# Kernel tuning notes

Measured on AMD Instinct MI355X. Metric: run time of the kernel, lower is better.

The kernel has to match this reference:

```python
import jax, jax.numpy as jnp
import numpy as np

B, NIMG, H, W, C = 4, 4, 80, 80, 256
NH = 8
C1 = C // 8          # 32
CPH = C1 // NH       # 4 per-head conv channels
K2D = 4              # deformable attention sampling points
HD2 = C1 // NH       # 4 head dim for 2D deformable attention
INNER = 32           # 3D deformable attention inner dim
DSF = (2, 8, 8)
OSC = jnp.array([2.0, 8.0, 8.0], jnp.float32)


def _bilin2d(img, px, py):
    # img [B,C,H,W]; px,py [B,K] pixel coords -> [B,K,C], zero-padded outside
    Bb, Cc, Hh, Ww = img.shape
    x0 = jnp.floor(px); y0 = jnp.floor(py)
    wx = px - x0; wy = py - y0
    bidx = jnp.arange(Bb)[:, None]
    def g(yy, xx):
        valid = (xx >= 0) & (xx <= Ww - 1) & (yy >= 0) & (yy <= Hh - 1)
        xi = jnp.clip(xx, 0, Ww - 1).astype(jnp.int32)
        yi = jnp.clip(yy, 0, Hh - 1).astype(jnp.int32)
        return img[bidx, :, yi, xi] * valid[..., None]
    return (g(y0, x0) * ((1 - wy) * (1 - wx))[..., None]
          + g(y0, x0 + 1) * ((1 - wy) * wx)[..., None]
          + g(y0 + 1, x0) * (wy * (1 - wx))[..., None]
          + g(y0 + 1, x0 + 1) * (wy * wx)[..., None])


def _trilin(img, z, y, x):
    # img [B,C,D,H,W]; z,y,x [B,K] -> [B,K,C]
    Bb, Cc, Dd, Hh, Ww = img.shape
    z0 = jnp.floor(z); y0 = jnp.floor(y); x0 = jnp.floor(x)
    wz = z - z0; wy = y - y0; wx = x - x0
    bidx = jnp.arange(Bb)[:, None]
    def g(zz, yy, xx):
        valid = (zz >= 0) & (zz <= Dd - 1) & (yy >= 0) & (yy <= Hh - 1) & (xx >= 0) & (xx <= Ww - 1)
        zi = jnp.clip(zz, 0, Dd - 1).astype(jnp.int32)
        yi = jnp.clip(yy, 0, Hh - 1).astype(jnp.int32)
        xi = jnp.clip(xx, 0, Ww - 1).astype(jnp.int32)
        return img[bidx, :, zi, yi, xi] * valid[..., None]
    out = 0.
    for dz in (0., 1.):
        for dy in (0., 1.):
            for dx in (0., 1.):
                w = ((1 - wz) if dz == 0. else wz) * ((1 - wy) if dy == 0. else wy) * ((1 - wx) if dx == 0. else wx)
                out = out + g(z0 + dz, y0 + dy, x0 + dx) * w[..., None]
    return out


def _fwd(x, W_qkv, b_qkv, W_fc, b_fc, W_doff, b_doff, W_dep, b_dep, W_st, b_st,
         W_off2d, b_off2d, W_attw, b_attw, W_val, b_val, W_out2d, b_out2d,
         W_q3, b_q3, W_k3, b_k3, W_v3, b_v3, W_offA, b_offA, W_offB, b_offB,
         W_out3, b_out3, rate1, rate2, nimg):
    xb = jnp.transpose(x, (1, 0, 2))                       # [B, nHW, C]
    Bb = xb.shape[0]
    qkv = xb @ W_qkv + b_qkv                               # [B, nHW, 2*C1]
    # ---------- deformable-conv (ACMix) branch ----------
    f_all = qkv.reshape(Bb, nimg * H * W, 2 * NH, CPH).transpose(0, 2, 1, 3)
    f9 = jnp.einsum('oc,bcnk->bonk', W_fc, f_all) + b_fc[None, :, None, None]
    f_conv = f9.transpose(0, 3, 1, 2).reshape(Bb, 9 * CPH, nimg, H, W)
    fin = f_conv.transpose(0, 2, 1, 3, 4).reshape(Bb * nimg, 9 * CPH, H, W)
    off = jax.lax.conv_general_dilated(fin, W_doff, (1, 1), ((1, 1), (1, 1)),
          dimension_numbers=('NCHW', 'OIHW', 'NCHW')) + b_doff[None, :, None, None]
    off = off.reshape(Bb * nimg, 9, 2, H, W)               # (dy,dx) per 3x3 tap
    hh, ww = jnp.meshgrid(jnp.arange(H, dtype=jnp.float32), jnp.arange(W, dtype=jnp.float32), indexing='ij')
    tap = jnp.arange(9)
    ky = (tap // 3 - 1).astype(jnp.float32); kx = (tap % 3 - 1).astype(jnp.float32)
    py = hh[None, None] + ky[None, :, None, None] + off[:, :, 0]
    px = ww[None, None] + kx[None, :, None, None] + off[:, :, 1]
    samp = _bilin2d(fin, px.reshape(Bb * nimg, -1), py.reshape(Bb * nimg, -1))
    samp = samp.reshape(Bb * nimg, 9, H, W, 9 * CPH).transpose(0, 4, 1, 2, 3)
    sg = samp.reshape(Bb * nimg, CPH, 9, 9, H, W)          # [Bn, g, cin_pg, taps, H, W]
    wg = W_dep.reshape(CPH, 27, 9, 9)                      # [g, out_pg, cin_pg, taps]
    dep = jnp.einsum('bgikhw,goik->bgohw', sg, wg).reshape(Bb * nimg, 27 * CPH, H, W) + b_dep[None, :, None, None]
    oc = dep.reshape(Bb, nimg, 27 * CPH, H, W).transpose(0, 2, 1, 3, 4)
    st_in = oc.reshape(Bb, CPH, 27, nimg, H, W)
    st = jnp.einsum('bginhw,goi->bgonhw', st_in, W_st).reshape(Bb, C, nimg, H, W) + b_st[None, :, None, None, None]
    out_conv = st.transpose(2, 3, 4, 0, 1).reshape(nimg * H * W, Bb, C)
    # ---------- per-frame 2D deformable attention ----------
    qk = qkv.reshape(Bb, nimg, H, W, 2, C1)
    q2 = qk[..., 0, :].reshape(Bb * nimg, H, W, C1)
    k2 = qk[..., 1, :].reshape(Bb * nimg, H, W, C1)
    gy, gx = jnp.meshgrid(jnp.arange(H, dtype=jnp.float32) / (H - 1),
                          jnp.arange(W, dtype=jnp.float32) / (W - 1), indexing='ij')
    ref = jnp.stack([gx, gy], -1)                          # [H,W,2] normalized (x,y)
    off2 = (q2 @ W_off2d + b_off2d).reshape(Bb * nimg, H, W, NH, K2D, 2)
    attw = jax.nn.softmax((q2 @ W_attw + b_attw).reshape(Bb * nimg, H, W, NH, K2D), axis=-1)
    v2 = (k2 @ W_val + b_val).reshape(Bb * nimg, H, W, NH, HD2)
    vimg = v2.transpose(0, 3, 4, 1, 2).reshape(Bb * nimg * NH, HD2, H, W)
    loc = ref[None, :, :, None, None, :] + off2 / jnp.array([W, H], jnp.float32)
    ppx = (loc[..., 0] * (W - 1)).transpose(0, 3, 1, 2, 4).reshape(Bb * nimg * NH, H * W * K2D)
    ppy = (loc[..., 1] * (H - 1)).transpose(0, 3, 1, 2, 4).reshape(Bb * nimg * NH, H * W * K2D)
    s2 = _bilin2d(vimg, ppx, ppy).reshape(Bb * nimg, NH, H, W, K2D, HD2)
    a2 = jnp.einsum('bhwnk,bnhwkd->bhwnd', attw, s2).reshape(Bb * nimg, H, W, C1)
    a2 = (a2 @ W_out2d + b_out2d).reshape(Bb, nimg, H, W, C1)
    # faithful reproduction of the source's frame-concat bug: frames [0,0,1,...,nimg-2]
    idx = jnp.array([0] + list(range(nimg - 1)))
    x3 = a2[:, idx].transpose(0, 4, 1, 2, 3)               # [B, C1, nimg, H, W]
    # ---------- 3D deformable attention ----------
    q3 = jnp.einsum('oc,bcnhw->bonhw', W_q3, x3) + b_q3[None, :, None, None, None]
    hid = jax.lax.conv_general_dilated(q3, W_offA, DSF, ((1, 1), (1, 1), (1, 1)),
          dimension_numbers=('NCDHW', 'OIDHW', 'NCDHW')) + b_offA[None, :, None, None, None]
    hid = jax.nn.gelu(hid)
    off3 = jnp.einsum('oc,bcnhw->bonhw', W_offB, hid) + b_offB[None, :, None, None, None]
    off3 = jnp.tanh(off3) * OSC[None, :, None, None, None]
    npr, hpr, wpr = off3.shape[2], off3.shape[3], off3.shape[4]
    gz, gy2, gx2 = jnp.meshgrid(jnp.arange(npr, dtype=jnp.float32) * 2 + 0.5,
                                jnp.arange(hpr, dtype=jnp.float32) * 8 + 3.5,
                                jnp.arange(wpr, dtype=jnp.float32) * 8 + 3.5, indexing='ij')
    cz = (gz[None] + off3[:, 0]).reshape(Bb, -1)
    cy = (gy2[None] + off3[:, 1]).reshape(Bb, -1)
    cx = (gx2[None] + off3[:, 2]).reshape(Bb, -1)
    kf = jnp.einsum('oc,bcnhw->bonhw', W_k3, x3) + b_k3[None, :, None, None, None]
    vf = jnp.einsum('oc,bcnhw->bonhw', W_v3, x3) + b_v3[None, :, None, None, None]
    ks_ = _trilin(kf, cz, cy, cx)                          # [B, L, INNER]
    vs_ = _trilin(vf, cz, cy, cx)
    qf = q3.reshape(Bb, INNER, -1).transpose(0, 2, 1)      # [B, N, INNER]
    at = jax.nn.softmax(jnp.einsum('bnd,bld->bnl', qf, ks_) * (INNER ** -0.5), axis=-1)
    o3 = jnp.einsum('bnl,bld->bnd', at, vs_).transpose(0, 2, 1).reshape(Bb, INNER, nimg, H, W)
    o3 = jnp.einsum('oc,bcnhw->bonhw', W_out3, o3) + b_out3[None, :, None, None, None]
    xattn = o3.transpose(2, 3, 4, 0, 1).reshape(nimg * H * W, Bb, C)
    return rate1 * xattn + rate2 * out_conv


def _p(key, shape, s=0.02):
    return jax.random.normal(key, shape, jnp.float32) * s


def setup_inputs() -> dict:
    key = jax.random.key(0)
    ks = jax.random.split(key, 20)
    z = lambda *s: jnp.zeros(s, jnp.float32)
    return {
        'x': jax.random.normal(ks[0], (NIMG * H * W, B, C), jnp.float32),
        'W_qkv': _p(ks[1], (C, C // 4)), 'b_qkv': z(C // 4),
        'W_fc': _p(ks[2], (9, 2 * NH)), 'b_fc': z(9),
        'W_doff': _p(ks[3], (18, 9 * CPH, 3, 3), 0.01), 'b_doff': z(18),
        'W_dep': _p(ks[4], (27 * CPH, 9, 3, 3)), 'b_dep': z(27 * CPH),
        'W_st': _p(ks[5], (CPH, C // CPH, 27)), 'b_st': z(C),
        'W_off2d': _p(ks[6], (C1, NH * K2D * 2), 0.01), 'b_off2d': z(NH * K2D * 2),
        'W_attw': _p(ks[7], (C1, NH * K2D)), 'b_attw': z(NH * K2D),
        'W_val': _p(ks[8], (C1, C1)), 'b_val': z(C1),
        'W_out2d': _p(ks[9], (C1, C1)), 'b_out2d': z(C1),
        'W_q3': _p(ks[10], (INNER, C1)), 'b_q3': z(INNER),
        'W_k3': _p(ks[11], (INNER, C1)), 'b_k3': z(INNER),
        'W_v3': _p(ks[12], (INNER, C1)), 'b_v3': z(INNER),
        'W_offA': _p(ks[13], (INNER, INNER, 4, 10, 10), 0.01), 'b_offA': z(INNER),
        'W_offB': _p(ks[14], (3, INNER), 0.01), 'b_offB': z(3),
        'W_out3': _p(ks[15], (C, INNER)), 'b_out3': z(C),
        'rate1': jnp.full((1,), 0.5, jnp.float32),
        'rate2': jnp.full((1,), 0.5, jnp.float32),
        'nimg': NIMG,
    }


def reference(x, W_qkv, b_qkv, W_fc, b_fc, W_doff, b_doff, W_dep, b_dep, W_st, b_st,
              W_off2d, b_off2d, W_attw, b_attw, W_val, b_val, W_out2d, b_out2d,
              W_q3, b_q3, W_k3, b_k3, W_v3, b_v3, W_offA, b_offA, W_offB, b_offB,
              W_out3, b_out3, rate1, rate2, nimg):
    return _fwd(x, W_qkv, b_qkv, W_fc, b_fc, W_doff, b_doff, W_dep, b_dep, W_st, b_st,
                W_off2d, b_off2d, W_attw, b_attw, W_val, b_val, W_out2d, b_out2d,
                W_q3, b_q3, W_k3, b_k3, W_v3, b_v3, W_offA, b_offA, W_offB, b_offB,
                W_out3, b_out3, rate1, rate2, nimg)
```

## Files before the change

kernel.cpp:

```cpp
#include <hip/hip_runtime.h>
#include <math.h>

#define B_     4
#define NIMG_  4
#define H_     80
#define W_     80
#define C_     256
#define NH_    8
#define HW_    6400
#define NQ_    25600
#define NPIX_  102400
#define L3_    200

#define WS_QH   0u
#define WS_KH   3276800u
#define WS_V2   6553600u
#define WS_FIN2 9830400u
#define WS_OFF  3276800u
#define WS_A2   9830400u
#define WS_Q3   0u
#define WS_KF   3276800u
#define WS_VF   6553600u
#define WS_CRD  9830400u
#define WS_KS   9832800u
#define WS_VS   9858400u
#define WS_O3   3276800u

__global__ __launch_bounds__(256) void k_qkv(const float* __restrict__ x,
        const float* __restrict__ Wq, const float* __restrict__ bq,
        float* __restrict__ qh, float* __restrict__ kh) {
    __shared__ __align__(16) float xs[32][256];
    int t = threadIdx.x;
    int row0 = blockIdx.x * 32;
    for (int it = 0; it < 8; ++it) {
        int idx = t + it * 256;
        int r = idx >> 6;
        int f4 = idx & 63;
        int row = row0 + r;
        int b = row / NQ_, n = row % NQ_;
        const float4* src = (const float4*)(x + ((size_t)n * B_ + b) * C_);
        ((float4*)&xs[r][0])[f4] = src[f4];
    }
    __syncthreads();
    int j = t & 63;
    int rbase = (t >> 6) * 8;
    float acc[8];
    #pragma unroll
    for (int r = 0; r < 8; ++r) acc[r] = 0.f;
    for (int c4 = 0; c4 < 64; ++c4) {
        float w0 = Wq[(c4 * 4 + 0) * 64 + j];
        float w1 = Wq[(c4 * 4 + 1) * 64 + j];
        float w2 = Wq[(c4 * 4 + 2) * 64 + j];
        float w3 = Wq[(c4 * 4 + 3) * 64 + j];
        #pragma unroll
        for (int r = 0; r < 8; ++r) {
            float4 xv = ((const float4*)&xs[rbase + r][0])[c4];
            acc[r] += xv.x * w0 + xv.y * w1 + xv.z * w2 + xv.w * w3;
        }
    }
    float bias = bq[j];
    #pragma unroll
    for (int r = 0; r < 8; ++r) {
        int row = row0 + rbase + r;
        float vres = acc[r] + bias;
        if (j < 32) qh[(size_t)row * 32 + j] = vres;
        else        kh[(size_t)row * 32 + (j - 32)] = vres;
    }
}

__global__ __launch_bounds__(256) void k_fin_v2(const float* __restrict__ qh,
        const float* __restrict__ kh,
        const float* __restrict__ Wfc, const float* __restrict__ bfc,
        const float* __restrict__ Wval, const float* __restrict__ bval,
        float* __restrict__ fin2, float* __restrict__ v2) {
    __shared__ float WvalL[1024], WfcL[144], bfcL[9], bvalL[32];
    int t = threadIdx.x;
    for (int d = t; d < 1024; d += 256) WvalL[d] = Wval[d];
    if (t < 144) WfcL[t] = Wfc[t];
    if (t >= 160 && t < 169) bfcL[t - 160] = bfc[t - 160];
    if (t >= 192 && t < 224) bvalL[t - 192] = bval[t - 192];
    __syncthreads();
    int P = blockIdx.x * 256 + t;
    int b = P / NQ_, nq = P % NQ_;
    int n = nq / HW_, hw = nq % HW_;
    int bn = b * NIMG_ + n;
    float q[64];
    const float4* qp = (const float4*)(qh + (size_t)P * 32);
    const float4* kp = (const float4*)(kh + (size_t)P * 32);
    #pragma unroll
    for (int i = 0; i < 8; ++i) ((float4*)q)[i] = qp[i];
    #pragma unroll
    for (int i = 0; i < 8; ++i) ((float4*)q)[8 + i] = kp[i];
    float fo[36];
    #pragma unroll
    for (int k = 0; k < 4; ++k)
        #pragma unroll
        for (int o = 0; o < 9; ++o) fo[k * 9 + o] = bfcL[o];
    for (int c = 0; c < 16; ++c) {
        #pragma unroll
        for (int o = 0; o < 9; ++o) {
            float wv = WfcL[o * 16 + c];
            #pragma unroll
            for (int k = 0; k < 4; ++k) fo[k * 9 + o] += wv * q[c * 4 + k];
        }
    }
    float* fp = fin2 + ((size_t)bn * HW_ + hw) * 48;
    #pragma unroll
    for (int g = 0; g < 4; ++g) {
        ((float4*)fp)[g * 3 + 0] = make_float4(fo[g * 9 + 0], fo[g * 9 + 1], fo[g * 9 + 2], fo[g * 9 + 3]);
        ((float4*)fp)[g * 3 + 1] = make_float4(fo[g * 9 + 4], fo[g * 9 + 5], fo[g * 9 + 6], fo[g * 9 + 7]);
        ((float4*)fp)[g * 3 + 2] = make_float4(fo[g * 9 + 8], 0.f, 0.f, 0.f);
    }
    float vo[32];
    #pragma unroll
    for (int j = 0; j < 32; ++j) vo[j] = bvalL[j];
    for (int c = 0; c < 32; ++c) {
        float qc = q[32 + c];
        #pragma unroll
        for (int j = 0; j < 32; ++j) vo[j] += qc * WvalL[c * 32 + j];
    }
    float* vp = v2 + ((size_t)bn * HW_ + hw) * 32;
    #pragma unroll
    for (int i = 0; i < 8; ++i) ((float4*)vp)[i] = ((float4*)vo)[i];
}

__global__ __launch_bounds__(256) void k_offconv(const float* __restrict__ fin2,
        const float* __restrict__ Wdoff, const float* __restrict__ bdoff,
        float* __restrict__ off) {
    __shared__ float Wl[5832];
    int t = threadIdx.x;
    for (int d = t; d < 5832; d += 256) {
        int tap = d / 648, r = d % 648, c = r / 18, o = r % 18;
        Wl[d] = Wdoff[(o * 36 + c) * 9 + tap];
    }
    __syncthreads();
    int P = blockIdx.x * 256 + t;
    int bn = P / HW_, hw = P % HW_;
    int h = hw / W_, w = hw % W_;
    float acc[18];
    #pragma unroll
    for (int o = 0; o < 18; ++o) acc[o] = bdoff[o];
    for (int ky = 0; ky < 3; ++ky) {
        int hh = h + ky - 1;
        if (hh < 0 || hh >= H_) continue;
        for (int kx = 0; kx < 3; ++kx) {
            int ww = w + kx - 1;
            if (ww < 0 || ww >= W_) continue;
            int sp = hh * W_ + ww;
            const float4* base = (const float4*)(fin2 + ((size_t)bn * HW_ + sp) * 48);
            const float* wl = Wl + (ky * 3 + kx) * 648;
            #pragma unroll
            for (int g = 0; g < 4; ++g) {
                float4 p0 = base[g * 3 + 0], p1 = base[g * 3 + 1], p2 = base[g * 3 + 2];
                float vals[9] = {p0.x, p0.y, p0.z, p0.w, p1.x, p1.y, p1.z, p1.w, p2.x};
                #pragma unroll
                for (int idx = 0; idx < 9; ++idx) {
                    const float* w0 = wl + (g * 9 + idx) * 18;
                    float vv = vals[idx];
                    #pragma unroll
                    for (int o = 0; o < 18; ++o) acc[o] += vv * w0[o];
                }
            }
        }
    }
    float* op = off + (size_t)P * 18;
    #pragma unroll
    for (int o = 0; o < 18; ++o) op[o] = acc[o];
}

__global__ __launch_bounds__(256, 4) void k_depst(const float* __restrict__ fin2,
        const float* __restrict__ off, const float* __restrict__ Wdep,
        const float* __restrict__ bdep, const float* __restrict__ Wst,
        const float* __restrict__ bst, const float* __restrict__ rate2p,
        float* __restrict__ out) {
    __shared__ __align__(16) float wdepL[2268];
    __shared__ __align__(16) float wstL[1728];
    __shared__ float bdepL[27];
    __shared__ float bstL[64];
    int t = threadIdx.x;
    int bx = blockIdx.x;
    int u = (bx & 7) * 200 + (bx >> 3);
    int chunk = u >> 2, g = u & 3;
    for (int d = t; d < 2268; d += 256) {
        int k = d / 252, r2 = d % 252;
        int i = r2 / 28, o = r2 % 28;
        wdepL[d] = (o < 27) ? Wdep[(size_t)(g * 27 + o) * 81 + i * 9 + k] : 0.f;
    }
    for (int d = t; d < 1728; d += 256) {
        int i = d >> 6, o = d & 63;
        wstL[d] = Wst[g * 1728 + o * 27 + i];
    }
    if (t < 27) bdepL[t] = bdep[g * 27 + t];
    if (t >= 32 && t < 96) bstL[t - 32] = bst[g * 64 + (t - 32)];
    __syncthreads();
    int P = chunk * 256 + t;
    int bn = P / HW_, hw = P % HW_;
    int h = hw / W_, w = hw % W_;
    int b = bn >> 2, n = bn & 3;
    const float* finb = fin2 + (size_t)bn * (HW_ * 48) + g * 12;
    float2 offs[9];
    {
        const float2* op2 = (const float2*)(off + (size_t)P * 18);
        #pragma unroll
        for (int k = 0; k < 9; ++k) offs[k] = op2[k];
    }
    float acc[27];
    #pragma unroll
    for (int o = 0; o < 27; ++o) acc[o] = 0.f;
    float hf = (float)h, wf = (float)w;
    #pragma unroll 1
    for (int k = 0; k < 9; ++k) {
        float py = hf + (float)(k / 3 - 1) + offs[k].x;
        float px = wf + (float)(k % 3 - 1) + offs[k].y;
        float y0f = floorf(py), x0f = floorf(px);
        float wy = py - y0f, wx = px - x0f;
        float wy0 = 1.f - wy, wx0 = 1.f - wx;
        float vy0 = (y0f >= 0.f && y0f <= 79.f) ? 1.f : 0.f;
        float vy1 = (y0f >= -1.f && y0f <= 78.f) ? 1.f : 0.f;
        float vx0 = (x0f >= 0.f && x0f <= 79.f) ? 1.f : 0.f;
        float vx1 = (x0f >= -1.f && x0f <= 78.f) ? 1.f : 0.f;
        int yi0 = (int)fminf(fmaxf(y0f, 0.f), 79.f);
        int yi1 = (int)fminf(fmaxf(y0f + 1.f, 0.f), 79.f);
        int xi0 = (int)fminf(fmaxf(x0f, 0.f), 79.f);
        int xi1 = (int)fminf(fmaxf(x0f + 1.f, 0.f), 79.f);
        float w00 = wy0 * wx0 * vy0 * vx0;
        float w01 = wy0 * wx  * vy0 * vx1;
        float w10 = wy  * wx0 * vy1 * vx0;
        float w11 = wy  * wx  * vy1 * vx1;
        const float4* c00 = (const float4*)(finb + (size_t)(yi0 * W_ + xi0) * 48);
        const float4* c01 = (const float4*)(finb + (size_t)(yi0 * W_ + xi1) * 48);
        const float4* c10 = (const float4*)(finb + (size_t)(yi1 * W_ + xi0) * 48);
        const float4* c11 = (const float4*)(finb + (size_t)(yi1 * W_ + xi1) * 48);
        float s[9];
        {
            float4 p0 = c00[0], p1 = c00[1], p2 = c00[2];
            s[0] = w00 * p0.x; s[1] = w00 * p0.y; s[2] = w00 * p0.z; s[3] = w00 * p0.w;
            s[4] = w00 * p1.x; s[5] = w00 * p1.y; s[6] = w00 * p1.z; s[7] = w00 * p1.w;
            s[8] = w00 * p2.x;
        }
        {
            float4 p0 = c01[0], p1 = c01[1], p2 = c01[2];
            s[0] += w01 * p0.x; s[1] += w01 * p0.y; s[2] += w01 * p0.z; s[3] += w01 * p0.w;
            s[4] += w01 * p1.x; s[5] += w01 * p1.y; s[6] += w01 * p1.z; s[7] += w01 * p1.w;
            s[8] += w01 * p2.x;
        }
        {
            float4 p0 = c10[0], p1 = c10[1], p2 = c10[2];
            s[0] += w10 * p0.x; s[1] += w10 * p0.y; s[2] += w10 * p0.z; s[3] += w10 * p0.w;
            s[4] += w10 * p1.x; s[5] += w10 * p1.y; s[6] += w10 * p1.z; s[7] += w10 * p1.w;
            s[8] += w10 * p2.x;
        }
        {
            float4 p0 = c11[0], p1 = c11[1], p2 = c11[2];
            s[0] += w11 * p0.x; s[1] += w11 * p0.y; s[2] += w11 * p0.z; s[3] += w11 * p0.w;
            s[4] += w11 * p1.x; s[5] += w11 * p1.y; s[6] += w11 * p1.z; s[7] += w11 * p1.w;
            s[8] += w11 * p2.x;
        }
        const float* wk = wdepL + k * 252;
        #pragma unroll
        for (int i = 0; i < 9; ++i) {
            float si = s[i];
            const float4* rw = (const float4*)(wk + i * 28);
            float4 q0 = rw[0], q1 = rw[1], q2 = rw[2], q3v = rw[3];
            float4 q4 = rw[4], q5 = rw[5], q6 = rw[6];
            acc[0]  += si * q0.x;  acc[1]  += si * q0.y;  acc[2]  += si * q0.z;  acc[3]  += si * q0.w;
            acc[4]  += si * q1.x;  acc[5]  += si * q1.y;  acc[6]  += si * q1.z;  acc[7]  += si * q1.w;
            acc[8]  += si * q2.x;  acc[9]  += si * q2.y;  acc[10] += si * q2.z;  acc[11] += si * q2.w;
            acc[12] += si * q3v.x; acc[13] += si * q3v.y; acc[14] += si * q3v.z; acc[15] += si * q3v.w;
            acc[16] += si * q4.x;  acc[17] += si * q4.y;  acc[18] += si * q4.z;  acc[19] += si * q4.w;
            acc[20] += si * q5.x;  acc[21] += si * q5.y;  acc[22] += si * q5.z;  acc[23] += si * q5.w;
            acc[24] += si * q6.x;  acc[25] += si * q6.y;  acc[26] += si * q6.z;
        }
    }
    #pragma unroll
    for (int i = 0; i < 27; ++i) acc[i] += bdepL[i];
    float r2v = rate2p[0];
    float* ob = out + ((size_t)(n * HW_ + hw) * B_ + b) * C_ + g * 64;
    #pragma unroll 1
    for (int half = 0; half < 2; ++half) {
        float ro[32];
        #pragma unroll
        for (int o = 0; o < 32; ++o) ro[o] = bstL[half * 32 + o];
        #pragma unroll
        for (int i = 0; i < 27; ++i) {
            float ai = acc[i];
            const float4* rw = (const float4*)(wstL + i * 64 + half * 32);
            #pragma unroll
            for (int j = 0; j < 8; ++j) {
                float4 wv = rw[j];
                ro[j * 4 + 0] += ai * wv.x;
                ro[j * 4 + 1] += ai * wv.y;
                ro[j * 4 + 2] += ai * wv.z;
                ro[j * 4 + 3] += ai * wv.w;
            }
        }
        float4* obv = (float4*)(ob + half * 32);
        #pragma unroll
        for (int o4 = 0; o4 < 8; ++o4)
            obv[o4] = make_float4(r2v * ro[o4 * 4 + 0], r2v * ro[o4 * 4 + 1],
                                  r2v * ro[o4 * 4 + 2], r2v * ro[o4 * 4 + 3]);
    }
}

__global__ __launch_bounds__(256) void k_attn2d(const float* __restrict__ qh,
        const float* __restrict__ v2,
        const float* __restrict__ Woff, const float* __restrict__ boff,
        const float* __restrict__ Watt, const float* __restrict__ batt,
        const float* __restrict__ Wout, const float* __restrict__ bout,
        float* __restrict__ a2) {
    __shared__ float WoffL[2048], WattL[1024], WoutL[1024];
    __shared__ float boffL[64], battL[32], boutL[32];
    int t = threadIdx.x;
    for (int d = t; d < 2048; d += 256) WoffL[d] = Woff[d];
    for (int d = t; d < 1024; d += 256) { WattL[d] = Watt[d]; WoutL[d] = Wout[d]; }
    if (t < 64) boffL[t] = boff[t];
    else if (t < 96) battL[t - 64] = batt[t - 64];
    else if (t < 128) boutL[t - 96] = bout[t - 96];
    __syncthreads();
    int P = blockIdx.x * 256 + t;
    int b = P / NQ_, nq = P % NQ_;
    int n = nq / HW_, hw = nq % HW_;
    int h = hw / W_, w = hw % W_;
    int bn = b * NIMG_ + n;
    float q[32];
    const float4* qp = (const float4*)(qh + (size_t)P * 32);
    #pragma unroll
    for (int i = 0; i < 8; ++i) ((float4*)q)[i] = qp[i];
    const float* vbase = v2 + (size_t)bn * HW_ * 32;
    float a2v[32];
    #pragma unroll
    for (int i = 0; i < 32; ++i) a2v[i] = 0.f;
    for (int nh = 0; nh < 8; ++nh) {
        float t0 = battL[nh * 4 + 0], t1 = battL[nh * 4 + 1];
        float t2 = battL[nh * 4 + 2], t3 = battL[nh * 4 + 3];
        for (int c = 0; c < 32; ++c) {
            float qc = q[c];
            const float* wr = WattL + c * 32 + nh * 4;
            t0 += qc * wr[0]; t1 += qc * wr[1]; t2 += qc * wr[2]; t3 += qc * wr[3];
        }
        float m = fmaxf(fmaxf(t0, t1), fmaxf(t2, t3));
        float e0 = expf(t0 - m), e1 = expf(t1 - m), e2 = expf(t2 - m), e3 = expf(t3 - m);
        float inv = 1.f / (e0 + e1 + e2 + e3);
        float pk[4] = {e0 * inv, e1 * inv, e2 * inv, e3 * inv};
        #pragma unroll
        for (int kk = 0; kk < 4; ++kk) {
            int j0 = nh * 8 + kk * 2;
            float ox = boffL[j0], oy = boffL[j0 + 1];
            for (int c = 0; c < 32; ++c) {
                float qc = q[c];
                ox += qc * WoffL[c * 64 + j0];
                oy += qc * WoffL[c * 64 + j0 + 1];
            }
            float ppx = (float)w + ox * (79.f / 80.f);
            float ppy = (float)h + oy * (79.f / 80.f);
            float x0 = floorf(ppx), y0 = floorf(ppy);
            float wx = ppx - x0, wy = ppy - y0;
            float s0 = 0.f, s1 = 0.f, s2 = 0.f, s3 = 0.f;
            #pragma unroll
            for (int cy = 0; cy < 2; ++cy) {
                float yf = y0 + (float)cy;
                if (yf < 0.f || yf > 79.f) continue;
                float wyf = cy ? wy : 1.f - wy;
                int yi = (int)yf;
                #pragma unroll
                for (int cx = 0; cx < 2; ++cx) {
                    float xf = x0 + (float)cx;
                    if (xf < 0.f || xf > 79.f) continue;
                    float wgt = wyf * (cx ? wx : 1.f - wx);
                    int xi = (int)xf;
                    float4 vv = *(const float4*)(vbase + ((size_t)yi * W_ + xi) * 32 + nh * 4);
                    s0 += wgt * vv.x; s1 += wgt * vv.y; s2 += wgt * vv.z; s3 += wgt * vv.w;
                }
            }
            float p = pk[kk];
            a2v[nh * 4 + 0] += p * s0; a2v[nh * 4 + 1] += p * s1;
            a2v[nh * 4 + 2] += p * s2; a2v[nh * 4 + 3] += p * s3;
        }
    }
    float ro[32];
    #pragma unroll
    for (int o = 0; o < 32; ++o) ro[o] = boutL[o];
    for (int c = 0; c < 32; ++c) {
        float ac = a2v[c];
        const float* wr = WoutL + c * 32;
        #pragma unroll
        for (int o = 0; o < 32; ++o) ro[o] += ac * wr[o];
    }
    float* op = a2 + ((size_t)bn * HW_ + hw) * 32;
    #pragma unroll
    for (int i = 0; i < 8; ++i) ((float4*)op)[i] = ((float4*)ro)[i];
}

__global__ __launch_bounds__(256) void k_qkv3(const float* __restrict__ a2,
        const float* __restrict__ Wq3, const float* __restrict__ bq3,
        const float* __restrict__ Wk3, const float* __restrict__ bk3,
        const float* __restrict__ Wv3, const float* __restrict__ bv3,
        float* __restrict__ q3, float* __restrict__ kf, float* __restrict__ vf) {
    __shared__ float Wq3L[1024], Wk3L[1024], Wv3L[1024];
    __shared__ float bq3L[32], bk3L[32], bv3L[32];
    int t = threadIdx.x;
    for (int d = t; d < 1024; d += 256) {
        Wq3L[d] = Wq3[d]; Wk3L[d] = Wk3[d]; Wv3L[d] = Wv3[d];
    }
    if (t < 32) { bq3L[t] = bq3[t]; bk3L[t] = bk3[t]; bv3L[t] = bv3[t]; }
    __syncthreads();
    int idx = blockIdx.x * 256 + t;
    int bn = idx / HW_, hw = idx % HW_;
    int b = bn >> 2, n = bn & 3;
    int ns = (n == 0) ? 0 : n - 1;
    const float* src = a2 + ((size_t)(b * 4 + ns) * HW_ + hw) * 32;
    float v[32];
    #pragma unroll
    for (int i = 0; i < 8; ++i) ((float4*)v)[i] = ((const float4*)src)[i];
    float oq[32], ok[32], ov[32];
    #pragma unroll
    for (int o = 0; o < 32; ++o) {
        float aq = bq3L[o], ak = bk3L[o], av = bv3L[o];
        #pragma unroll
        for (int c = 0; c < 32; ++c) {
            aq += Wq3L[o * 32 + c] * v[c];
            ak += Wk3L[o * 32 + c] * v[c];
            av += Wv3L[o * 32 + c] * v[c];
        }
        oq[o] = aq; ok[o] = ak; ov[o] = av;
    }
    float* qo = q3 + (size_t)idx * 32;
    float* ko = kf + (size_t)idx * 32;
    float* vo = vf + (size_t)idx * 32;
    #pragma unroll
    for (int i = 0; i < 8; ++i) {
        ((float4*)qo)[i] = ((float4*)oq)[i];
        ((float4*)ko)[i] = ((float4*)ok)[i];
        ((float4*)vo)[i] = ((float4*)ov)[i];
    }
}

__global__ __launch_bounds__(256) void k_offs3d(const float* __restrict__ q3,
        const float* __restrict__ WoffA, const float* __restrict__ boffA,
        const float* __restrict__ WoffB, const float* __restrict__ boffB,
        float* __restrict__ coords) {
    __shared__ float red[4][128];
    __shared__ float hidl[128];
    int t = threadIdx.x;
    int blk = blockIdx.x;
    int zo = blk / 100, r = blk % 100, ho = r / 10, wo = r % 10;
    float acc[4][32];
    #pragma unroll
    for (int b = 0; b < 4; ++b)
        #pragma unroll
        for (int o = 0; o < 32; ++o) acc[b][o] = 0.f;
    for (int tap = t; tap < 400; tap += 256) {
        int kz = tap / 100, r2 = tap % 100, ky = r2 / 10, kx = r2 % 10;
        int zi = zo * 2 + kz - 1, hi = ho * 8 + ky - 1, wi = wo * 8 + kx - 1;
        if (zi < 0 || zi >= NIMG_ || hi < 0 || hi >= H_ || wi < 0 || wi >= W_) continue;
        const float* wb = WoffA + tap;
        int sp = hi * W_ + wi;
        for (int c = 0; c < 32; ++c) {
            float vb[4];
            #pragma unroll
            for (int b = 0; b < 4; ++b)
                vb[b] = q3[((size_t)(b * 4 + zi) * HW_ + sp) * 32 + c];
            #pragma unroll
            for (int o = 0; o < 32; ++o) {
                float wv = wb[(o * 32 + c) * 400];
                #pragma unroll
                for (int b = 0; b < 4; ++b) acc[b][o] += vb[b] * wv;
            }
        }
    }
    #pragma unroll
    for (int b = 0; b < 4; ++b)
        #pragma unroll
        for (int o = 0; o < 32; ++o)
            for (int sh = 32; sh >= 1; sh >>= 1)
                acc[b][o] += __shfl_xor(acc[b][o], sh);
    int lane = t & 63, wv = t >> 6;
    if (lane == 0)
        for (int b = 0; b < 4; ++b)
            for (int o = 0; o < 32; ++o) red[wv][b * 32 + o] = acc[b][o];
    __syncthreads();
    if (t < 128) {
        float v = red[0][t] + red[1][t] + red[2][t] + red[3][t] + boffA[t & 31];
        float v3 = v * v * v;
        hidl[t] = 0.5f * v * (1.f + tanhf(0.7978845608028654f * (v + 0.044715f * v3)));
    }
    __syncthreads();
    if (t < 12) {
        int b = t / 3, j = t % 3;
        float a = boffB[j];
        for (int o = 0; o < 32; ++o) a += WoffB[j * 32 + o] * hidl[b * 32 + o];
        float osc = (j == 0) ? 2.f : 8.f;
        float base = (j == 0) ? (zo * 2 + 0.5f) : ((j == 1) ? (ho * 8 + 3.5f) : (wo * 8 + 3.5f));
        coords[((size_t)b * L3_ + blk) * 3 + j] = base + tanhf(a) * osc;
    }
}

__global__ __launch_bounds__(256) void k_trisample(const float* __restrict__ kf,
        const float* __restrict__ vf, const float* __restrict__ coords,
        float* __restrict__ ks, float* __restrict__ vs) {
    int t = threadIdx.x;
    int wv = blockIdx.x * 4 + (t >> 6);
    int b = wv / L3_, l = wv % L3_;
    int lane = t & 63;
    int c = lane & 31;
    const float* src = (lane < 32) ? kf : vf;
    float* dst = (lane < 32) ? ks : vs;
    const float* cp = coords + ((size_t)b * L3_ + l) * 3;
    float cz = cp[0], cy = cp[1], cx = cp[2];
    float z0 = floorf(cz), y0 = floorf(cy), x0 = floorf(cx);
    float wz = cz - z0, wy = cy - y0, wx = cx - x0;
    float acc = 0.f;
    #pragma unroll
    for (int dz = 0; dz < 2; ++dz) {
        float zf = z0 + (float)dz;
        if (zf < 0.f || zf > 3.f) continue;
        float wzf = dz ? wz : 1.f - wz;
        int zi = (int)zf;
        #pragma unroll
        for (int dy = 0; dy < 2; ++dy) {
            float yf = y0 + (float)dy;
            if (yf < 0.f || yf > 79.f) continue;
            float wyf = wzf * (dy ? wy : 1.f - wy);
            int yi = (int)yf;
            #pragma unroll
            for (int dx = 0; dx < 2; ++dx) {
                float xf = x0 + (float)dx;
                if (xf < 0.f || xf > 79.f) continue;
                float wgt = wyf * (dx ? wx : 1.f - wx);
                int xi = (int)xf;
                acc += wgt * src[((size_t)(b * 4 + zi) * HW_ + yi * W_ + xi) * 32 + c];
            }
        }
    }
    dst[((size_t)b * L3_ + l) * 32 + c] = acc;
}

__global__ __launch_bounds__(256) void k_attn3d(const float* __restrict__ q3,
        const float* __restrict__ ks, const float* __restrict__ vs,
        float* __restrict__ o3) {
    __shared__ __align__(16) float ksl[L3_ * 32];
    __shared__ __align__(16) float vsl[L3_ * 32];
    int t = threadIdx.x;
    int b = blockIdx.x / 100;
    int chunk = blockIdx.x % 100;
    const float4* ksg = (const float4*)(ks + (size_t)b * L3_ * 32);
    const float4* vsg = (const float4*)(vs + (size_t)b * L3_ * 32);
    for (int d = t; d < L3_ * 8; d += 256) {
        ((float4*)ksl)[d] = ksg[d];
        ((float4*)vsl)[d] = vsg[d];
    }
    __syncthreads();
    int N = chunk * 256 + t;
    float q[32];
    const float4* qp = (const float4*)(q3 + ((size_t)b * NQ_ + N) * 32);
    #pragma unroll
    for (int i = 0; i < 8; ++i) ((float4*)q)[i] = qp[i];
    const float scale = 0.17677669529663687f;
    float den = 0.f;
    float o[32];
    #pragma unroll
    for (int c = 0; c < 32; ++c) o[c] = 0.f;
    for (int l = 0; l < L3_; ++l) {
        const float4* kp = (const float4*)(ksl + l * 32);
        float s = 0.f;
        #pragma unroll
        for (int c4 = 0; c4 < 8; ++c4) {
            float4 kv = kp[c4];
            s += q[c4 * 4 + 0] * kv.x + q[c4 * 4 + 1] * kv.y + q[c4 * 4 + 2] * kv.z + q[c4 * 4 + 3] * kv.w;
        }
        float p = expf(s * scale);
        den += p;
        const float4* vp = (const float4*)(vsl + l * 32);
        #pragma unroll
        for (int c4 = 0; c4 < 8; ++c4) {
            float4 vv = vp[c4];
            o[c4 * 4 + 0] += p * vv.x; o[c4 * 4 + 1] += p * vv.y;
            o[c4 * 4 + 2] += p * vv.z; o[c4 * 4 + 3] += p * vv.w;
        }
    }
    float inv = 1.f / den;
    float* op = o3 + ((size_t)b * NQ_ + N) * 32;
    #pragma unroll
    for (int c = 0; c < 32; ++c) op[c] = o[c] * inv;
}

__global__ __launch_bounds__(256) void k_final(const float* __restrict__ o3,
        const float* __restrict__ W, const float* __restrict__ bias,
        const float* __restrict__ r1p, float* __restrict__ out) {
    __shared__ float o3T[32 * 128];
    __shared__ float WT[32 * 260];
    int t = threadIdx.x;
    int R0 = blockIdx.x * 128;
    {
        int row = t >> 1, k0 = (t & 1) * 16;
        int R = R0 + row;
        int b = R & 3, N = R >> 2;
        const float* src = o3 + ((size_t)b * NQ_ + N) * 32 + k0;
        #pragma unroll
        for (int j = 0; j < 16; ++j) o3T[(k0 + j) * 128 + row] = src[j];
    }
    for (int d = t; d < 8192; d += 256) {
        int c = d >> 5, k = d & 31;
        WT[k * 260 + c] = W[d];
    }
    __syncthreads();
    int tc = t & 15;
    int tr = t >> 4;
    int r0 = tr * 8;
    float acc[8][16];
    #pragma unroll
    for (int i = 0; i < 8; ++i)
        #pragma unroll
        for (int j = 0; j < 16; ++j) acc[i][j] = 0.f;
    #pragma unroll 1
    for (int k = 0; k < 32; ++k) {
        float a[8];
        *(float4*)&a[0] = *(const float4*)&o3T[k * 128 + r0];
        *(float4*)&a[4] = *(const float4*)&o3T[k * 128 + r0 + 4];
        float wv[16];
        #pragma unroll
        for (int ci = 0; ci < 16; ++ci) wv[ci] = WT[k * 260 + tc + 16 * ci];
        #pragma unroll
        for (int i = 0; i < 8; ++i)
            #pragma unroll
            for (int j = 0; j < 16; ++j) acc[i][j] += a[i] * wv[j];
    }
    float r1 = r1p[0];
    float bs[16];
    #pragma unroll
    for (int ci = 0; ci < 16; ++ci) bs[ci] = bias[tc + 16 * ci];
    #pragma unroll 1
    for (int i = 0; i < 8; ++i) {
        size_t rowbase = (size_t)(R0 + r0 + i) * 256;
        #pragma unroll
        for (int j = 0; j < 16; ++j) {
            size_t oi = rowbase + tc + 16 * j;
            out[oi] = r1 * (acc[i][j] + bs[j]) + out[oi];
        }
    }
}

extern "C" void kernel_launch(void* const* d_in, const int* in_sizes, int n_in,
                              void* d_out, int out_size, void* d_ws, size_t ws_size,
                              hipStream_t stream) {
    (void)in_sizes; (void)n_in; (void)out_size; (void)ws_size;
    const float* x      = (const float*)d_in[0];
    const float* W_qkv  = (const float*)d_in[1];
    const float* b_qkv  = (const float*)d_in[2];
    const float* W_fc   = (const float*)d_in[3];
    const float* b_fc   = (const float*)d_in[4];
    const float* W_doff = (const float*)d_in[5];
    const float* b_doff = (const float*)d_in[6];
    const float* W_dep  = (const float*)d_in[7];
    const float* b_dep  = (const float*)d_in[8];
    const float* W_st   = (const float*)d_in[9];
    const float* b_st   = (const float*)d_in[10];
    const float* W_off2d= (const float*)d_in[11];
    const float* b_off2d= (const float*)d_in[12];
    const float* W_attw = (const float*)d_in[13];
    const float* b_attw = (const float*)d_in[14];
    const float* W_val  = (const float*)d_in[15];
    const float* b_val  = (const float*)d_in[16];
    const float* W_out2d= (const float*)d_in[17];
    const float* b_out2d= (const float*)d_in[18];
    const float* W_q3   = (const float*)d_in[19];
    const float* b_q3   = (const float*)d_in[20];
    const float* W_k3   = (const float*)d_in[21];
    const float* b_k3   = (const float*)d_in[22];
    const float* W_v3   = (const float*)d_in[23];
    const float* b_v3   = (const float*)d_in[24];
    const float* W_offA = (const float*)d_in[25];
    const float* b_offA = (const float*)d_in[26];
    const float* W_offB = (const float*)d_in[27];
    const float* b_offB = (const float*)d_in[28];
    const float* W_out3 = (const float*)d_in[29];
    const float* b_out3 = (const float*)d_in[30];
    const float* rate1  = (const float*)d_in[31];
    const float* rate2  = (const float*)d_in[32];

    float* ws  = (float*)d_ws;
    float* out = (float*)d_out;
    float* qhp = ws + WS_QH;
    float* khp = ws + WS_KH;
    float* fn2 = ws + WS_FIN2;
    float* off = ws + WS_OFF;
    float* v2  = ws + WS_V2;
    float* a2  = ws + WS_A2;
    float* q3  = ws + WS_Q3;
    float* kf  = ws + WS_KF;
    float* vf  = ws + WS_VF;
    float* crd = ws + WS_CRD;
    float* ks  = ws + WS_KS;
    float* vs  = ws + WS_VS;
    float* o3w = ws + WS_O3;

    k_qkv      <<<3200,   256, 0, stream>>>(x, W_qkv, b_qkv, qhp, khp);
    k_fin_v2   <<<400,    256, 0, stream>>>(qhp, khp, W_fc, b_fc, W_val, b_val, fn2, v2);
    k_offconv  <<<400,    256, 0, stream>>>(fn2, W_doff, b_doff, off);
    k_depst    <<<1600,   256, 0, stream>>>(fn2, off, W_dep, b_dep, W_st, b_st, rate2, out);
    k_attn2d   <<<400,    256, 0, stream>>>(qhp, v2, W_off2d, b_off2d, W_attw, b_attw, W_out2d, b_out2d, a2);
    k_qkv3     <<<400,    256, 0, stream>>>(a2, W_q3, b_q3, W_k3, b_k3, W_v3, b_v3, q3, kf, vf);
    k_offs3d   <<<200,    256, 0, stream>>>(q3, W_offA, b_offA, W_offB, b_offB, crd);
    k_trisample<<<200,    256, 0, stream>>>(kf, vf, crd, ks, vs);
    k_attn3d   <<<400,    256, 0, stream>>>(q3, ks, vs, o3w);
    k_final    <<<800,    256, 0, stream>>>(o3w, W_out3, b_out3, rate1, out);
}
```

Baseline: 886.5 us.

## Split per-pixel work across 4 threads in offconv, attn2d and qkv3

Three per-pixel kernels (offset conv, 2D deformable attention, 3D qkv projection) now assign four threads per pixel instead of one. Each thread handles a quarter of the channel groups, heads or outputs, and partial sums are combined with xor shuffles where needed. Grids grow from 400 to 1600 blocks to expose more parallelism and cut per-thread register pressure on the 102400-pixel launches. The cost is redundant index math, per-thread reloads of q, extra shuffles and less coalesced partial stores. The bilinear sampling in depst is also moved into a helper function as a refactor.

Result: slower. 985.1 us (+11.1%).

```diff
diff --git a/kernel.cpp b/kernel.cpp
--- a/kernel.cpp
+++ b/kernel.cpp
@@ -26,6 +26,53 @@
 #define WS_VS   9858400u
 #define WS_O3   3276800u
 
+__device__ __forceinline__ void bilin9(const float* __restrict__ finb,
+        float py, float px, float* __restrict__ s) {
+    float y0f = floorf(py), x0f = floorf(px);
+    float wy = py - y0f, wx = px - x0f;
+    float wy0 = 1.f - wy, wx0 = 1.f - wx;
+    float vy0 = (y0f >= 0.f && y0f <= 79.f) ? 1.f : 0.f;
+    float vy1 = (y0f >= -1.f && y0f <= 78.f) ? 1.f : 0.f;
+    float vx0 = (x0f >= 0.f && x0f <= 79.f) ? 1.f : 0.f;
+    float vx1 = (x0f >= -1.f && x0f <= 78.f) ? 1.f : 0.f;
+    int yi0 = (int)fminf(fmaxf(y0f, 0.f), 79.f);
+    int yi1 = (int)fminf(fmaxf(y0f + 1.f, 0.f), 79.f);
+    int xi0 = (int)fminf(fmaxf(x0f, 0.f), 79.f);
+    int xi1 = (int)fminf(fmaxf(x0f + 1.f, 0.f), 79.f);
+    float w00 = wy0 * wx0 * vy0 * vx0;
+    float w01 = wy0 * wx  * vy0 * vx1;
+    float w10 = wy  * wx0 * vy1 * vx0;
+    float w11 = wy  * wx  * vy1 * vx1;
+    const float4* c00 = (const float4*)(finb + (size_t)(yi0 * W_ + xi0) * 48);
+    const float4* c01 = (const float4*)(finb + (size_t)(yi0 * W_ + xi1) * 48);
+    const float4* c10 = (const float4*)(finb + (size_t)(yi1 * W_ + xi0) * 48);
+    const float4* c11 = (const float4*)(finb + (size_t)(yi1 * W_ + xi1) * 48);
+    {
+        float4 p0 = c00[0], p1 = c00[1], p2 = c00[2];
+        s[0] = w00 * p0.x; s[1] = w00 * p0.y; s[2] = w00 * p0.z; s[3] = w00 * p0.w;
+        s[4] = w00 * p1.x; s[5] = w00 * p1.y; s[6] = w00 * p1.z; s[7] = w00 * p1.w;
+        s[8] = w00 * p2.x;
+    }
+    {
+        float4 p0 = c01[0], p1 = c01[1], p2 = c01[2];
+        s[0] += w01 * p0.x; s[1] += w01 * p0.y; s[2] += w01 * p0.z; s[3] += w01 * p0.w;
+        s[4] += w01 * p1.x; s[5] += w01 * p1.y; s[6] += w01 * p1.z; s[7] += w01 * p1.w;
+        s[8] += w01 * p2.x;
+    }
+    {
+        float4 p0 = c10[0], p1 = c10[1], p2 = c10[2];
+        s[0] += w10 * p0.x; s[1] += w10 * p0.y; s[2] += w10 * p0.z; s[3] += w10 * p0.w;
+        s[4] += w10 * p1.x; s[5] += w10 * p1.y; s[6] += w10 * p1.z; s[7] += w10 * p1.w;
+        s[8] += w10 * p2.x;
+    }
+    {
+        float4 p0 = c11[0], p1 = c11[1], p2 = c11[2];
+        s[0] += w11 * p0.x; s[1] += w11 * p0.y; s[2] += w11 * p0.z; s[3] += w11 * p0.w;
+        s[4] += w11 * p1.x; s[5] += w11 * p1.y; s[6] += w11 * p1.z; s[7] += w11 * p1.w;
+        s[8] += w11 * p2.x;
+    }
+}
+
 __global__ __launch_bounds__(256) void k_qkv(const float* __restrict__ x,
         const float* __restrict__ Wq, const float* __restrict__ bq,
         float* __restrict__ qh, float* __restrict__ kh) {
@@ -134,12 +181,13 @@
         Wl[d] = Wdoff[(o * 36 + c) * 9 + tap];
     }
     __syncthreads();
-    int P = blockIdx.x * 256 + t;
+    int P = blockIdx.x * 64 + (t >> 2);
+    int g = t & 3;
     int bn = P / HW_, hw = P % HW_;
     int h = hw / W_, w = hw % W_;
     float acc[18];
     #pragma unroll
-    for (int o = 0; o < 18; ++o) acc[o] = bdoff[o];
+    for (int o = 0; o < 18; ++o) acc[o] = (g == 0) ? bdoff[o] : 0.f;
     for (int ky = 0; ky < 3; ++ky) {
         int hh = h + ky - 1;
         if (hh < 0 || hh >= H_) continue;
@@ -147,25 +195,30 @@
             int ww = w + kx - 1;
             if (ww < 0 || ww >= W_) continue;
             int sp = hh * W_ + ww;
-            const float4* base = (const float4*)(fin2 + ((size_t)bn * HW_ + sp) * 48);
-            const float* wl = Wl + (ky * 3 + kx) * 648;
+            const float4* base = (const float4*)(fin2 + ((size_t)bn * HW_ + sp) * 48 + g * 12);
+            float4 p0 = base[0], p1 = base[1], p2 = base[2];
+            float vals[9] = {p0.x, p0.y, p0.z, p0.w, p1.x, p1.y, p1.z, p1.w, p2.x};
+            const float* wl = Wl + (ky * 3 + kx) * 648 + g * 9 * 18;
             #pragma unroll
-            for (int g = 0; g < 4; ++g) {
-                float4 p0 = base[g * 3 + 0], p1 = base[g * 3 + 1], p2 = base[g * 3 + 2];
-                float vals[9] = {p0.x, p0.y, p0.z, p0.w, p1.x, p1.y, p1.z, p1.w, p2.x};
+            for (int idx = 0; idx < 9; ++idx) {
+                const float* w0 = wl + idx * 18;
+                float vv = vals[idx];
                 #pragma unroll
-                for (int idx = 0; idx < 9; ++idx) {
-                    const float* w0 = wl + (g * 9 + idx) * 18;
-                    float vv = vals[idx];
-                    #pragma unroll
-                    for (int o = 0; o < 18; ++o) acc[o] += vv * w0[o];
-                }
+                for (int o = 0; o < 18; ++o) acc[o] += vv * w0[o];
             }
         }
     }
-    float* op = off + (size_t)P * 18;
-    #pragma unroll
-    for (int o = 0; o < 18; ++o) op[o] = acc[o];
+    #pragma unroll
+    for (int o = 0; o < 18; ++o) {
+        acc[o] += __shfl_xor(acc[o], 1);
+        acc[o] += __shfl_xor(acc[o], 2);
+    }
+    if (g == 0) {
+        float2* op = (float2*)(off + (size_t)P * 18);
+        #pragma unroll
+        for (int o2 = 0; o2 < 9; ++o2)
+            op[o2] = make_float2(acc[o2 * 2], acc[o2 * 2 + 1]);
+    }
 }
 
 __global__ __launch_bounds__(256, 4) void k_depst(const float* __restrict__ fin2,
@@ -212,50 +265,8 @@
     for (int k = 0; k < 9; ++k) {
         float py = hf + (float)(k / 3 - 1) + offs[k].x;
         float px = wf + (float)(k % 3 - 1) + offs[k].y;
-        float y0f = floorf(py), x0f = floorf(px);
-        float wy = py - y0f, wx = px - x0f;
-        float wy0 = 1.f - wy, wx0 = 1.f - wx;
-        float vy0 = (y0f >= 0.f && y0f <= 79.f) ? 1.f : 0.f;
-        float vy1 = (y0f >= -1.f && y0f <= 78.f) ? 1.f : 0.f;
-        float vx0 = (x0f >= 0.f && x0f <= 79.f) ? 1.f : 0.f;
-        float vx1 = (x0f >= -1.f && x0f <= 78.f) ? 1.f : 0.f;
-        int yi0 = (int)fminf(fmaxf(y0f, 0.f), 79.f);
-        int yi1 = (int)fminf(fmaxf(y0f + 1.f, 0.f), 79.f);
-        int xi0 = (int)fminf(fmaxf(x0f, 0.f), 79.f);
-        int xi1 = (int)fminf(fmaxf(x0f + 1.f, 0.f), 79.f);
-        float w00 = wy0 * wx0 * vy0 * vx0;
-        float w01 = wy0 * wx  * vy0 * vx1;
-        float w10 = wy  * wx0 * vy1 * vx0;
-        float w11 = wy  * wx  * vy1 * vx1;
-        const float4* c00 = (const float4*)(finb + (size_t)(yi0 * W_ + xi0) * 48);
-        const float4* c01 = (const float4*)(finb + (size_t)(yi0 * W_ + xi1) * 48);
-        const float4* c10 = (const float4*)(finb + (size_t)(yi1 * W_ + xi0) * 48);
-        const float4* c11 = (const float4*)(finb + (size_t)(yi1 * W_ + xi1) * 48);
         float s[9];
-        {
-            float4 p0 = c00[0], p1 = c00[1], p2 = c00[2];
-            s[0] = w00 * p0.x; s[1] = w00 * p0.y; s[2] = w00 * p0.z; s[3] = w00 * p0.w;
-            s[4] = w00 * p1.x; s[5] = w00 * p1.y; s[6] = w00 * p1.z; s[7] = w00 * p1.w;
-            s[8] = w00 * p2.x;
-        }
-        {
-            float4 p0 = c01[0], p1 = c01[1], p2 = c01[2];
-            s[0] += w01 * p0.x; s[1] += w01 * p0.y; s[2] += w01 * p0.z; s[3] += w01 * p0.w;
-            s[4] += w01 * p1.x; s[5] += w01 * p1.y; s[6] += w01 * p1.z; s[7] += w01 * p1.w;
-            s[8] += w01 * p2.x;
-        }
-        {
-            float4 p0 = c10[0], p1 = c10[1], p2 = c10[2];
-            s[0] += w10 * p0.x; s[1] += w10 * p0.y; s[2] += w10 * p0.z; s[3] += w10 * p0.w;
-            s[4] += w10 * p1.x; s[5] += w10 * p1.y; s[6] += w10 * p1.z; s[7] += w10 * p1.w;
-            s[8] += w10 * p2.x;
-        }
-        {
-            float4 p0 = c11[0], p1 = c11[1], p2 = c11[2];
-            s[0] += w11 * p0.x; s[1] += w11 * p0.y; s[2] += w11 * p0.z; s[3] += w11 * p0.w;
-            s[4] += w11 * p1.x; s[5] += w11 * p1.y; s[6] += w11 * p1.z; s[7] += w11 * p1.w;
-            s[8] += w11 * p2.x;
-        }
+        bilin9(finb, py, px, s);
         const float* wk = wdepL + k * 252;
         #pragma unroll
         for (int i = 0; i < 9; ++i) {
@@ -308,8 +319,8 @@
         const float* __restrict__ Watt, const float* __restrict__ batt,
         const float* __restrict__ Wout, const float* __restrict__ bout,
         float* __restrict__ a2) {
-    __shared__ float WoffL[2048], WattL[1024], WoutL[1024];
-    __shared__ float boffL[64], battL[32], boutL[32];
+    __shared__ __align__(16) float WoffL[2048], WattL[1024], WoutL[1024];
+    __shared__ __align__(16) float boffL[64], battL[32], boutL[32];
     int t = threadIdx.x;
     for (int d = t; d < 2048; d += 256) WoffL[d] = Woff[d];
     for (int d = t; d < 1024; d += 256) { WattL[d] = Watt[d]; WoutL[d] = Wout[d]; }
@@ -317,7 +328,8 @@
     else if (t < 96) battL[t - 64] = batt[t - 64];
     else if (t < 128) boutL[t - 96] = bout[t - 96];
     __syncthreads();
-    int P = blockIdx.x * 256 + t;
+    int P = blockIdx.x * 64 + (t >> 2);
+    int hp = t & 3;
     int b = P / NQ_, nq = P % NQ_;
     int n = nq / HW_, hw = nq % HW_;
     int h = hw / W_, w = hw % W_;
@@ -327,16 +339,18 @@
     #pragma unroll
     for (int i = 0; i < 8; ++i) ((float4*)q)[i] = qp[i];
     const float* vbase = v2 + (size_t)bn * HW_ * 32;
-    float a2v[32];
-    #pragma unroll
-    for (int i = 0; i < 32; ++i) a2v[i] = 0.f;
-    for (int nh = 0; nh < 8; ++nh) {
+    float av8[8];
+    #pragma unroll
+    for (int i = 0; i < 8; ++i) av8[i] = 0.f;
+    #pragma unroll
+    for (int u2 = 0; u2 < 2; ++u2) {
+        int nh = hp * 2 + u2;
         float t0 = battL[nh * 4 + 0], t1 = battL[nh * 4 + 1];
         float t2 = battL[nh * 4 + 2], t3 = battL[nh * 4 + 3];
         for (int c = 0; c < 32; ++c) {
             float qc = q[c];
-            const float* wr = WattL + c * 32 + nh * 4;
-            t0 += qc * wr[0]; t1 += qc * wr[1]; t2 += qc * wr[2]; t3 += qc * wr[3];
+            float4 wr = *(const float4*)(WattL + c * 32 + nh * 4);
+            t0 += qc * wr.x; t1 += qc * wr.y; t2 += qc * wr.z; t3 += qc * wr.w;
         }
         float m = fmaxf(fmaxf(t0, t1), fmaxf(t2, t3));
         float e0 = expf(t0 - m), e1 = expf(t1 - m), e2 = expf(t2 - m), e3 = expf(t3 - m);
@@ -348,8 +362,9 @@
             float ox = boffL[j0], oy = boffL[j0 + 1];
             for (int c = 0; c < 32; ++c) {
                 float qc = q[c];
-                ox += qc * WoffL[c * 64 + j0];
-                oy += qc * WoffL[c * 64 + j0 + 1];
+                float2 wv2 = *(const float2*)(WoffL + c * 64 + j0);
+                ox += qc * wv2.x;
+                oy += qc * wv2.y;
             }
             float ppx = (float)w + ox * (79.f / 80.f);
             float ppy = (float)h + oy * (79.f / 80.f);
@@ -373,22 +388,31 @@
                 }
             }
             float p = pk[kk];
-            a2v[nh * 4 + 0] += p * s0; a2v[nh * 4 + 1] += p * s1;
-            a2v[nh * 4 + 2] += p * s2; a2v[nh * 4 + 3] += p * s3;
+            av8[u2 * 4 + 0] += p * s0; av8[u2 * 4 + 1] += p * s1;
+            av8[u2 * 4 + 2] += p * s2; av8[u2 * 4 + 3] += p * s3;
         }
     }
     float ro[32];
     #pragma unroll
-    for (int o = 0; o < 32; ++o) ro[o] = boutL[o];
-    for (int c = 0; c < 32; ++c) {
-        float ac = a2v[c];
-        const float* wr = WoutL + c * 32;
+    for (int o = 0; o < 32; ++o) ro[o] = 0.f;
+    #pragma unroll
+    for (int j = 0; j < 8; ++j) {
+        float ac = av8[j];
+        const float* wr = WoutL + (hp * 8 + j) * 32;
         #pragma unroll
         for (int o = 0; o < 32; ++o) ro[o] += ac * wr[o];
     }
-    float* op = a2 + ((size_t)bn * HW_ + hw) * 32;
-    #pragma unroll
-    for (int i = 0; i < 8; ++i) ((float4*)op)[i] = ((float4*)ro)[i];
+    #pragma unroll
+    for (int o = 0; o < 32; ++o) {
+        ro[o] += __shfl_xor(ro[o], 1);
+        ro[o] += __shfl_xor(ro[o], 2);
+    }
+    float* op = a2 + ((size_t)bn * HW_ + hw) * 32 + hp * 8;
+    float outv[8];
+    #pragma unroll
+    for (int j = 0; j < 8; ++j) outv[j] = ro[hp * 8 + j] + boutL[hp * 8 + j];
+    ((float4*)op)[0] = ((float4*)outv)[0];
+    ((float4*)op)[1] = ((float4*)outv)[1];
 }
 
 __global__ __launch_bounds__(256) void k_qkv3(const float* __restrict__ a2,
@@ -396,7 +420,7 @@
         const float* __restrict__ Wk3, const float* __restrict__ bk3,
         const float* __restrict__ Wv3, const float* __restrict__ bv3,
         float* __restrict__ q3, float* __restrict__ kf, float* __restrict__ vf) {
-    __shared__ float Wq3L[1024], Wk3L[1024], Wv3L[1024];
+    __shared__ __align__(16) float Wq3L[1024], Wk3L[1024], Wv3L[1024];
     __shared__ float bq3L[32], bk3L[32], bv3L[32];
     int t = threadIdx.x;
     for (int d = t; d < 1024; d += 256) {
@@ -404,7 +428,8 @@
     }
     if (t < 32) { bq3L[t] = bq3[t]; bk3L[t] = bk3[t]; bv3L[t] = bv3[t]; }
     __syncthreads();
-    int idx = blockIdx.x * 256 + t;
+    int idx = blockIdx.x * 64 + (t >> 2);
+    int qq = t & 3;
     int bn = idx / HW_, hw = idx % HW_;
     int b = bn >> 2, n = bn & 3;
     int ns = (n == 0) ? 0 : n - 1;
@@ -412,9 +437,10 @@
     float v[32];
     #pragma unroll
     for (int i = 0; i < 8; ++i) ((float4*)v)[i] = ((const float4*)src)[i];
-    float oq[32], ok[32], ov[32];
-    #pragma unroll
-    for (int o = 0; o < 32; ++o) {
+    float oq[8], ok[8], ov[8];
+    #pragma unroll
+    for (int oo = 0; oo < 8; ++oo) {
+        int o = qq * 8 + oo;
         float aq = bq3L[o], ak = bk3L[o], av = bv3L[o];
         #pragma unroll
         for (int c = 0; c < 32; ++c) {
@@ -422,13 +448,13 @@
             ak += Wk3L[o * 32 + c] * v[c];
             av += Wv3L[o * 32 + c] * v[c];
         }
-        oq[o] = aq; ok[o] = ak; ov[o] = av;
-    }
-    float* qo = q3 + (size_t)idx * 32;
-    float* ko = kf + (size_t)idx * 32;
-    float* vo = vf + (size_t)idx * 32;
-    #pragma unroll
-    for (int i = 0; i < 8; ++i) {
+        oq[oo] = aq; ok[oo] = ak; ov[oo] = av;
+    }
+    float* qo = q3 + (size_t)idx * 32 + qq * 8;
+    float* ko = kf + (size_t)idx * 32 + qq * 8;
+    float* vo = vf + (size_t)idx * 32 + qq * 8;
+    #pragma unroll
+    for (int i = 0; i < 2; ++i) {
         ((float4*)qo)[i] = ((float4*)oq)[i];
         ((float4*)ko)[i] = ((float4*)ok)[i];
         ((float4*)vo)[i] = ((float4*)ov)[i];
@@ -696,10 +722,10 @@
 
     k_qkv      <<<3200,   256, 0, stream>>>(x, W_qkv, b_qkv, qhp, khp);
     k_fin_v2   <<<400,    256, 0, stream>>>(qhp, khp, W_fc, b_fc, W_val, b_val, fn2, v2);
-    k_offconv  <<<400,    256, 0, stream>>>(fn2, W_doff, b_doff, off);
+    k_offconv  <<<1600,   256, 0, stream>>>(fn2, W_doff, b_doff, off);
     k_depst    <<<1600,   256, 0, stream>>>(fn2, off, W_dep, b_dep, W_st, b_st, rate2, out);
-    k_attn2d   <<<400,    256, 0, stream>>>(qhp, v2, W_off2d, b_off2d, W_attw, b_attw, W_out2d, b_out2d, a2);
-    k_qkv3     <<<400,    256, 0, stream>>>(a2, W_q3, b_q3, W_k3, b_k3, W_v3, b_v3, q3, kf, vf);
+    k_attn2d   <<<1600,   256, 0, stream>>>(qhp, v2, W_off2d, b_off2d, W_attw, b_attw, W_out2d, b_out2d, a2);
+    k_qkv3     <<<1600,   256, 0, stream>>>(a2, W_q3, b_q3, W_k3, b_k3, W_v3, b_v3, q3, kf, vf);
     k_offs3d   <<<200,    256, 0, stream>>>(q3, W_offA, b_offA, W_offB, b_offB, crd);
     k_trisample<<<200,    256, 0, stream>>>(kf, vf, crd, ks, vs);
     k_attn3d   <<<400,    256, 0, stream>>>(q3, ks, vs, o3w);
```
